# Kernel optimization log

Hardware: AMD Instinct MI355X
Metric: run time of the kernel (lower is better)

Reference implementation:

```python
import jax, jax.numpy as jnp
import numpy as np

N_SUB = 60000   # nodes in current subgraph (rows of fnode/agraph/subnode)
M = 120000      # total messages (directed edges)
K = 8           # max neighbors per node/message
H = 128         # hidden_size
IN = 256        # input_size (fmess feature dim)
FD = 128        # node_fdim
DEPTH = 2       # rnn depth (sparse_forward iterations)
NUM_NODES = 65536


def setup_inputs() -> dict:
    key = jax.random.key(0)
    ks = jax.random.split(key, 12)
    s = 0.05
    def w(k, shape):
        return jax.random.normal(k, shape, jnp.float32) * s
    return {
        "fnode": jax.random.normal(ks[0], (N_SUB, FD), jnp.float32),
        "fmess": jax.random.normal(ks[1], (M, IN), jnp.float32),
        "agraph": jax.random.randint(ks[2], (N_SUB, K), 0, M, dtype=jnp.int32),
        "bgraph": jax.random.randint(ks[3], (M, K), 0, M, dtype=jnp.int32),
        "h_in": jax.random.normal(ks[4], (M, H), jnp.float32),
        "c_in": jax.random.normal(ks[5], (M, H), jnp.float32),
        "submess": jnp.arange(N_SUB, dtype=jnp.int32),
        "subnode": jnp.arange(N_SUB, dtype=jnp.int32),
        "num_nodes": NUM_NODES,
        # tree-LSTM gate weights, stored [in_dim, out_dim]
        "Wi": w(ks[6], (IN + H, H)), "bi": jnp.zeros((H,), jnp.float32),
        "Wo": w(ks[7], (IN + H, H)), "bo": jnp.zeros((H,), jnp.float32),
        "Wf": w(ks[8], (IN + H, H)), "bf": jnp.zeros((H,), jnp.float32),
        "Wu": w(ks[9], (IN + H, H)), "bu": jnp.zeros((H,), jnp.float32),
        # node readout W_o: Linear(node_fdim + hidden -> hidden) + ReLU (+ Dropout = eval no-op)
        "Wn": w(ks[10], (FD + H, H)), "bn": jnp.zeros((H,), jnp.float32),
    }


def _lstm_cell(x, h_nei, c_nei, Wi, bi, Wo, bo, Wf, bf, Wu, bu):
    # x: [S, IN]; h_nei, c_nei: [S, K, H]  (hgraph-style child-sum tree LSTM)
    h_sum = h_nei.sum(axis=1)                         # [S, H]
    z = jnp.concatenate([x, h_sum], axis=-1)          # [S, IN+H]
    i = jax.nn.sigmoid(z @ Wi + bi)
    o = jax.nn.sigmoid(z @ Wo + bo)
    u = jnp.tanh(z @ Wu + bu)
    # per-neighbor forget gate: sigmoid(cat([x_expand, h_nei]) @ Wf + bf),
    # split the matmul so we never materialize the [S, K, IN+H] concat
    d_in = x.shape[1]
    fx = x @ Wf[:d_in] + bf                           # [S, H]
    f = jax.nn.sigmoid(fx[:, None, :] + h_nei @ Wf[d_in:])  # [S, K, H]
    c = i * u + (f * c_nei).sum(axis=1)
    h = o * jnp.tanh(c)
    return h, c


def reference(fnode, fmess, agraph, bgraph, h_in, c_in, submess, subnode, num_nodes,
              Wi, bi, Wo, bo, Wf, bf, Wu, bu, Wn, bn):
    # LSTM.sparse_forward: zero state at submess rows, then iteratively update them
    mask = jnp.ones((h_in.shape[0],), h_in.dtype).at[submess].set(0.0)
    h = h_in * mask[:, None]
    c = c_in * mask[:, None]
    x_sub = fmess[submess]       # [S, IN]
    bg_sub = bgraph[submess]     # [S, K] message-neighbor ids
    for _ in range(DEPTH):
        h_nei = h[bg_sub]        # [S, K, H] gather
        c_nei = c[bg_sub]
        sub_h, sub_c = _lstm_cell(x_sub, h_nei, c_nei, Wi, bi, Wo, bo, Wf, bf, Wu, bu)
        h = h.at[submess].set(sub_h)   # index_scatter
        c = c.at[submess].set(sub_c)
    # node update: gather incoming messages, sum, Linear + ReLU (dropout inactive at eval)
    nei_message = h[agraph].sum(axis=1)                      # [N_SUB, H]
    node_hiddens = jnp.concatenate([fnode, nei_message], axis=-1)
    node_hiddens = jax.nn.relu(node_hiddens @ Wn + bn)       # [N_SUB, H]
    node_buf = jnp.zeros((num_nodes, node_hiddens.shape[1]), node_hiddens.dtype)
    node_buf = node_buf.at[subnode].set(node_hiddens)        # index_scatter into full buffer
    return node_buf, h, c
```

## Files before the change

### kernel.cpp

```cpp
#include <hip/hip_runtime.h>
#include <cstdint>
#include <cstddef>

#define Hc   128
#define INc  256
#define Kc   8
#define HP   136
#define HSP  136
#define EPH  136
#define ZP2  264

typedef unsigned short ushortT;
typedef __attribute__((ext_vector_type(8))) short bf16x8;
typedef __attribute__((ext_vector_type(4))) float f32x4;
typedef __attribute__((ext_vector_type(4))) unsigned short us4;
typedef __attribute__((ext_vector_type(8))) unsigned short us8;

__device__ __forceinline__ float fsig(float x) {
  return __builtin_amdgcn_rcpf(1.f + __expf(-x));
}
__device__ __forceinline__ float ftanh(float x) {
  float e = __expf(2.f * fminf(x, 15.f));
  return (e - 1.f) * __builtin_amdgcn_rcpf(e + 1.f);
}
__device__ __forceinline__ ushortT f2bf(float f) {
  unsigned u = __builtin_bit_cast(unsigned, f);
  unsigned r = (u + 0x7fffu + ((u >> 16) & 1u)) >> 16;
  return (ushortT)r;
}
__device__ __forceinline__ us4 f2bf4(float4 v) {
  us4 o; o[0] = f2bf(v.x); o[1] = f2bf(v.y); o[2] = f2bf(v.z); o[3] = f2bf(v.w);
  return o;
}
__device__ __forceinline__ float bf2f(ushortT u) {
  return __builtin_bit_cast(float, (unsigned)u << 16);
}

#define GATE_FRAGS (4*8*12*64)
#define WN_FRAGS   (8*8*64)

__global__ void marks_init(int* __restrict__ mark, int M, int* __restrict__ nmark, int NN) {
  int i = blockIdx.x * blockDim.x + threadIdx.x;
  if (i < M) mark[i] = -1;
  if (i < NN) nmark[i] = -1;
}

__global__ void set_repack(const int* __restrict__ submess, const int* __restrict__ subnode,
                           int S, int* __restrict__ mark, int* __restrict__ nmark,
                           const float* __restrict__ Wi, const float* __restrict__ Wo,
                           const float* __restrict__ Wu, const float* __restrict__ Wf,
                           const float* __restrict__ Wn, ushortT* __restrict__ pack, int SB) {
  if ((int)blockIdx.x < SB) {
    int i = blockIdx.x * 256 + threadIdx.x;
    if (i < S) { mark[submess[i]] = i; nmark[subnode[i]] = i; }
    return;
  }
  int idx = (blockIdx.x - SB) * 256 + threadIdx.x;
  if (idx < GATE_FRAGS) {
    int lane = idx & 63;
    int kt = (idx >> 6) % 12;
    int gc = idx / (64 * 12);
    int c = gc & 7, g = gc >> 3;
    const float* W = (g == 0) ? Wi : (g == 1) ? Wo : (g == 2) ? Wu : Wf;
    int k0 = kt * 32 + (lane >> 4) * 8;
    int col = c * 16 + (lane & 15);
    ushortT* dst = pack + (size_t)idx * 8;
    #pragma unroll
    for (int j = 0; j < 8; ++j) dst[j] = f2bf(W[(size_t)(k0 + j) * Hc + col]);
  } else if (idx < GATE_FRAGS + WN_FRAGS) {
    int i2 = idx - GATE_FRAGS;
    int lane = i2 & 63;
    int kt = (i2 >> 6) & 7;
    int c = i2 >> 9;
    int k0 = kt * 32 + (lane >> 4) * 8;
    int col = c * 16 + (lane & 15);
    ushortT* dst = pack + (size_t)GATE_FRAGS * 8 + (size_t)i2 * 8;
    #pragma unroll
    for (int j = 0; j < 8; ++j) dst[j] = f2bf(Wn[(size_t)(k0 + j) * Hc + col]);
  }
}

__device__ __forceinline__ const bf16x8* wh_frag(const ushortT* pack, int g, int cw, int kf, int lane) {
  return (const bf16x8*)&pack[(size_t)(((g * 8 + cw) * 12 + (8 + kf)) * 64 + lane) * 8];
}

__global__ __launch_bounds__(256) void stage_xg(
    const float* __restrict__ h_in, const float* __restrict__ c_in,
    const int* __restrict__ mark,
    float* __restrict__ h_out, float* __restrict__ c_out,
    ushortT* __restrict__ H16x, ushortT* __restrict__ C16x, ushortT* __restrict__ Hf16x,
    const float* __restrict__ fmess, const int* __restrict__ submess,
    const ushortT* __restrict__ pack,
    const float* __restrict__ bi, const float* __restrict__ bo,
    const float* __restrict__ bu, const float* __restrict__ bfb,
    ushortT* __restrict__ Xg, int M, int S, int stageBlocks)
{
  __shared__ __align__(16) ushortT xs[16 * ZP2];
  __shared__ int msr[16];
  const int t = threadIdx.x;

  if ((int)blockIdx.x < stageBlocks) {
    if (blockIdx.x == 0 && t < 48) {
      int arr = t >> 4, cp = t & 15;
      ushortT* dst = (arr == 0) ? H16x : (arr == 1) ? C16x : Hf16x;
      us8 z;
      #pragma unroll
      for (int e = 0; e < 8; ++e) z[e] = 0;
      *(us8*)&dst[(size_t)(M + S) * Hc + cp * 8] = z;
    }
    long total = (long)M * 16;
    for (long idx = (long)blockIdx.x * 256 + t; idx < total; idx += (long)stageBlocks * 256) {
      long j = idx >> 4;
      int cp = (int)(idx & 15);
      if (mark[j] >= 0) continue;
      const float4* h4 = (const float4*)(h_in + (size_t)j * Hc);
      const float4* c4 = (const float4*)(c_in + (size_t)j * Hc);
      float4 a0 = h4[cp * 2], a1 = h4[cp * 2 + 1];
      float4 b0 = c4[cp * 2], b1 = c4[cp * 2 + 1];
      ((float4*)(h_out + (size_t)j * Hc))[cp * 2] = a0;
      ((float4*)(h_out + (size_t)j * Hc))[cp * 2 + 1] = a1;
      ((float4*)(c_out + (size_t)j * Hc))[cp * 2] = b0;
      ((float4*)(c_out + (size_t)j * Hc))[cp * 2 + 1] = b1;
      *(us4*)&H16x[(size_t)j * Hc + cp * 8]     = f2bf4(a0);
      *(us4*)&H16x[(size_t)j * Hc + cp * 8 + 4] = f2bf4(a1);
      *(us4*)&C16x[(size_t)j * Hc + cp * 8]     = f2bf4(b0);
      *(us4*)&C16x[(size_t)j * Hc + cp * 8 + 4] = f2bf4(b1);
    }
    return;
  }

  const int row0 = (blockIdx.x - stageBlocks) * 16;
  if (t < 16) msr[t] = (row0 + t < S) ? submess[row0 + t] : -1;
  __syncthreads();
  {
    int r = t >> 4, cp = t & 15;
    int ms = msr[r];
    const float4* xr = (ms >= 0) ? (const float4*)(fmess + (size_t)ms * INc) : nullptr;
    #pragma unroll
    for (int q = 0; q < 4; ++q) {
      int slot = cp + q * 16;
      float4 v;
      if (xr) v = xr[slot]; else { v.x = v.y = v.z = v.w = 0.f; }
      *(us4*)&xs[r * ZP2 + slot * 4] = f2bf4(v);
    }
  }
  __syncthreads();

  const int w = t >> 6, lane = t & 63, lg = lane >> 4, cl = lane & 15;
  f32x4 acc[8];
  #pragma unroll
  for (int i = 0; i < 8; ++i) acc[i] = (f32x4){0.f, 0.f, 0.f, 0.f};
  const ushortT* zr = &xs[cl * ZP2 + lg * 8];
  #pragma unroll
  for (int kt = 0; kt < 8; ++kt) {
    bf16x8 a = *(const bf16x8*)&zr[kt * 32];
    #pragma unroll
    for (int c = 0; c < 8; ++c) {
      bf16x8 b = *(const bf16x8*)&pack[(size_t)(((w * 8 + c) * 12 + kt) * 64 + lane) * 8];
      acc[c] = __builtin_amdgcn_mfma_f32_16x16x32_bf16(a, b, acc[c], 0, 0, 0);
    }
  }
  const float* bias = (w == 0) ? bi : (w == 1) ? bo : (w == 2) ? bu : bfb;
  #pragma unroll
  for (int c = 0; c < 8; ++c) {
    int col = c * 16 + cl;
    float bv = bias[col];
    #pragma unroll
    for (int reg = 0; reg < 4; ++reg) {
      int s = row0 + lg * 4 + reg;
      if (s < S) Xg[(size_t)s * 512 + w * 128 + col] = f2bf(acc[c][reg] + bv);
    }
  }
}

__global__ __launch_bounds__(256) void hf_rows0(
    const ushortT* __restrict__ H16x, const int* __restrict__ mark,
    const ushortT* __restrict__ pack, ushortT* __restrict__ Hf16x, int M)
{
  __shared__ __align__(16) ushortT zh[16 * HP];
  __shared__ int mk[16];
  const int t = threadIdx.x;
  const int row0 = blockIdx.x * 16;

  if (t < 16) mk[t] = (row0 + t < M) ? mark[row0 + t] : 0;
  __syncthreads();
  {
    int r = t >> 4, cp = t & 15;
    us8 v;
    #pragma unroll
    for (int e = 0; e < 8; ++e) v[e] = 0;
    if (mk[r] < 0) v = *(const us8*)&H16x[(size_t)(row0 + r) * Hc + cp * 8];
    *(us8*)&zh[r * HP + cp * 8] = v;
  }
  __syncthreads();

  const int w = t >> 6, lane = t & 63, lg = lane >> 4, cl = lane & 15;
  f32x4 acc0 = (f32x4){0.f,0.f,0.f,0.f}, acc1 = acc0;
  const ushortT* zr = &zh[cl * HP + lg * 8];
  #pragma unroll
  for (int kf = 0; kf < 4; ++kf) {
    bf16x8 a = *(const bf16x8*)&zr[kf * 32];
    acc0 = __builtin_amdgcn_mfma_f32_16x16x32_bf16(a, *wh_frag(pack, 3, w*2+0, kf, lane), acc0, 0, 0, 0);
    acc1 = __builtin_amdgcn_mfma_f32_16x16x32_bf16(a, *wh_frag(pack, 3, w*2+1, kf, lane), acc1, 0, 0, 0);
  }
  #pragma unroll
  for (int half = 0; half < 2; ++half) {
    int col = (w * 2 + half) * 16 + cl;
    f32x4 a_ = half ? acc1 : acc0;
    #pragma unroll
    for (int reg = 0; reg < 4; ++reg) {
      int row = lg * 4 + reg;
      if (mk[row] < 0) Hf16x[(size_t)(row0 + row) * Hc + col] = f2bf(a_[reg]);
    }
  }
}

template<int MODE>
__global__ __launch_bounds__(256) void lstm8(
    const int* __restrict__ submess, const int* __restrict__ bgraph,
    const int* __restrict__ mark,
    ushortT* H16x, ushortT* C16x, ushortT* Hf16x,
    const ushortT* __restrict__ Xg, const ushortT* __restrict__ pack,
    ushortT* hsumNS, ushortT* cpartNS,
    float* __restrict__ dstH, float* __restrict__ dstC, int S, int M)
{
  __shared__ __align__(16) ushortT zs[16 * HSP];
  __shared__ __align__(16) ushortT pih[16 * EPH];
  __shared__ __align__(16) ushortT poh[16 * EPH];
  __shared__ __align__(16) ushortT puh[16 * EPH];
  __shared__ int nbj[16][Kc];
  __shared__ int msrow[16];

  const int t = threadIdx.x;
  const int row0 = blockIdx.x * 16;
  const int DUMMY = M + S;

  if (t < 128) {
    int r = t >> 3, k = t & 7;
    int s = row0 + r;
    int ms = (s < S) ? submess[s] : -1;
    if (k == 0) msrow[r] = ms;
    int j = DUMMY;
    if (ms >= 0) {
      int jj = bgraph[(size_t)ms * Kc + k];
      int m = mark[jj];
      j = (MODE == 0) ? (m >= 0 ? DUMMY : jj) : (m >= 0 ? M + m : DUMMY);
    }
    nbj[r][k] = j;
  }
  __syncthreads();

  {
    int r = t >> 4, cp = t & 15;
    int spos = row0 + r;
    float sum[8] = {0.f,0.f,0.f,0.f,0.f,0.f,0.f,0.f};
    if (MODE == 1 && spos < S) {
      us8 hs = *(const us8*)&hsumNS[(size_t)spos * Hc + cp * 8];
      #pragma unroll
      for (int e = 0; e < 8; ++e) sum[e] = bf2f(hs[e]);
    }
    #pragma unroll
    for (int k = 0; k < Kc; ++k) {
      int j = nbj[r][k];
      us8 v = *(const us8*)&H16x[(size_t)j * Hc + cp * 8];
      #pragma unroll
      for (int e = 0; e < 8; ++e) sum[e] += bf2f(v[e]);
    }
    us4 o0, o1;
    #pragma unroll
    for (int e = 0; e < 4; ++e) { o0[e] = f2bf(sum[e]); o1[e] = f2bf(sum[4 + e]); }
    *(us4*)&zs[r * HSP + cp * 8] = o0;
    *(us4*)&zs[r * HSP + cp * 8 + 4] = o1;
    if (MODE == 0 && spos < S) {
      *(us4*)&hsumNS[(size_t)spos * Hc + cp * 8] = o0;
      *(us4*)&hsumNS[(size_t)spos * Hc + cp * 8 + 4] = o1;
    }
  }
  __syncthreads();

  const int w = t >> 6, lane = t & 63, lg = lane >> 4, cl = lane & 15;

  f32x4 acc[6];
  #pragma unroll
  for (int i = 0; i < 6; ++i) acc[i] = (f32x4){0.f, 0.f, 0.f, 0.f};
  const ushortT* zrow = &zs[cl * HSP + lg * 8];
  #pragma unroll
  for (int kf = 0; kf < 4; ++kf) {
    bf16x8 a = *(const bf16x8*)&zrow[kf * 32];
    #pragma unroll
    for (int g = 0; g < 3; ++g)
      #pragma unroll
      for (int half = 0; half < 2; ++half)
        acc[g * 2 + half] = __builtin_amdgcn_mfma_f32_16x16x32_bf16(
            a, *wh_frag(pack, g, w * 2 + half, kf, lane), acc[g * 2 + half], 0, 0, 0);
  }

  #pragma unroll
  for (int half = 0; half < 2; ++half) {
    int col = (w * 2 + half) * 16 + cl;
    #pragma unroll
    for (int reg = 0; reg < 4; ++reg) {
      int row = lg * 4 + reg;
      pih[row * EPH + col] = f2bf(acc[0 + half][reg]);
      poh[row * EPH + col] = f2bf(acc[2 + half][reg]);
      puh[row * EPH + col] = f2bf(acc[4 + half][reg]);
    }
  }
  __syncthreads();

  {
    int r = t >> 4, cc = t & 15;
    int ms = msrow[r];
    int spos = row0 + r;
    const ushortT* xgr = Xg + (size_t)spos * 512 + cc * 8;
    us8 xi8 = *(const us8*)&xgr[0];
    us8 xo8 = *(const us8*)&xgr[128];
    us8 xu8 = *(const us8*)&xgr[256];
    us8 xf8 = *(const us8*)&xgr[384];
    us8 pi8 = *(const us8*)&pih[r * EPH + cc * 8];
    us8 po8 = *(const us8*)&poh[r * EPH + cc * 8];
    us8 pu8 = *(const us8*)&puh[r * EPH + cc * 8];
    float fx[8], ovv[8], iu[8], cn[8];
    #pragma unroll
    for (int e = 0; e < 8; ++e) {
      float iv = fsig(bf2f(xi8[e]) + bf2f(pi8[e]));
      float uv = ftanh(bf2f(xu8[e]) + bf2f(pu8[e]));
      ovv[e] = fsig(bf2f(xo8[e]) + bf2f(po8[e]));
      fx[e] = bf2f(xf8[e]);
      iu[e] = iv * uv;
      cn[e] = 0.f;
    }
    #pragma unroll
    for (int k = 0; k < Kc; ++k) {
      int j = nbj[r][k];
      us8 hf8 = *(const us8*)&Hf16x[(size_t)j * Hc + cc * 8];
      us8 cn8 = *(const us8*)&C16x[(size_t)j * Hc + cc * 8];
      #pragma unroll
      for (int e = 0; e < 8; ++e)
        cn[e] = fmaf(fsig(fx[e] + bf2f(hf8[e])), bf2f(cn8[e]), cn[e]);
    }
    float cacc[8];
    if (MODE == 1 && spos < S) {
      us8 cp8 = *(const us8*)&cpartNS[(size_t)spos * Hc + cc * 8];
      #pragma unroll
      for (int e = 0; e < 8; ++e) cacc[e] = iu[e] + cn[e] + bf2f(cp8[e]);
    } else {
      #pragma unroll
      for (int e = 0; e < 8; ++e) cacc[e] = iu[e] + cn[e];
    }
    float hv[8];
    #pragma unroll
    for (int e = 0; e < 8; ++e) hv[e] = ovv[e] * ftanh(cacc[e]);

    if (MODE == 0) {
      us8 h8, c8, cn16;
      #pragma unroll
      for (int e = 0; e < 8; ++e) {
        h8[e] = (spos < S) ? f2bf(hv[e]) : (ushortT)0;
        c8[e] = f2bf(cacc[e]);
        cn16[e] = f2bf(cn[e]);
      }
      if (spos < S) {
        *(us8*)&H16x[(size_t)(M + spos) * Hc + cc * 8] = h8;
        *(us8*)&C16x[(size_t)(M + spos) * Hc + cc * 8] = c8;
        *(us8*)&cpartNS[(size_t)spos * Hc + cc * 8] = cn16;
      }
      *(us4*)&zs[r * HSP + cc * 8]     = (us4){h8[0], h8[1], h8[2], h8[3]};
      *(us4*)&zs[r * HSP + cc * 8 + 4] = (us4){h8[4], h8[5], h8[6], h8[7]};
    } else {
      if (ms >= 0) {
        float* dh = dstH + (size_t)ms * Hc + cc * 8;
        float* dc = dstC + (size_t)ms * Hc + cc * 8;
        *(float4*)&dh[0] = *(float4*)&hv[0];
        *(float4*)&dh[4] = *(float4*)&hv[4];
        *(float4*)&dc[0] = *(float4*)&cacc[0];
        *(float4*)&dc[4] = *(float4*)&cacc[4];
      }
    }
  }

  if (MODE == 0) {
    __syncthreads();
    f32x4 a0 = (f32x4){0.f,0.f,0.f,0.f}, a1 = a0;
    const ushortT* zr2 = &zs[cl * HSP + lg * 8];
    #pragma unroll
    for (int kf = 0; kf < 4; ++kf) {
      bf16x8 a = *(const bf16x8*)&zr2[kf * 32];
      a0 = __builtin_amdgcn_mfma_f32_16x16x32_bf16(a, *wh_frag(pack, 3, w*2+0, kf, lane), a0, 0, 0, 0);
      a1 = __builtin_amdgcn_mfma_f32_16x16x32_bf16(a, *wh_frag(pack, 3, w*2+1, kf, lane), a1, 0, 0, 0);
    }
    #pragma unroll
    for (int half = 0; half < 2; ++half) {
      int col = (w * 2 + half) * 16 + cl;
      f32x4 a_ = half ? a1 : a0;
      #pragma unroll
      for (int reg = 0; reg < 4; ++reg) {
        int sp = row0 + lg * 4 + reg;
        if (sp < S) Hf16x[(size_t)(M + sp) * Hc + col] = f2bf(a_[reg]);
      }
    }
  }
}

__global__ __launch_bounds__(256) void readout_zero(
    const float* __restrict__ fnode, const int* __restrict__ agraph,
    const int* __restrict__ subnode, const float* __restrict__ h_out,
    const ushortT* __restrict__ H16x, const int* __restrict__ mark,
    const int* __restrict__ nmark,
    const ushortT* __restrict__ packWn, const float* __restrict__ bn,
    float* __restrict__ node_buf, int Nsub, int num_nodes, int NB, int ZB)
{
  __shared__ __align__(16) ushortT z2[16 * ZP2];
  __shared__ int orow[16];
  __shared__ int jn[16][Kc];

  const int t = threadIdx.x;

  if ((int)blockIdx.x >= NB) {
    long total = (long)num_nodes * 16;
    float4 z; z.x = z.y = z.z = z.w = 0.f;
    for (long idx = (long)(blockIdx.x - NB) * 256 + t; idx < total; idx += (long)ZB * 256) {
      long v = idx >> 4;
      int cp = (int)(idx & 15);
      if (nmark[v] < 0) {
        ((float4*)(node_buf + (size_t)v * Hc))[cp * 2] = z;
        ((float4*)(node_buf + (size_t)v * Hc))[cp * 2 + 1] = z;
      }
    }
    return;
  }

  const int row0 = blockIdx.x * 16;
  if (t < 16) orow[t] = (row0 + t < Nsub) ? subnode[row0 + t] : -1;
  if (t >= 64 && t < 64 + 128) {
    int i = t - 64, r = i >> 3, k = i & 7;
    int v = row0 + r;
    int j = 0;
    if (v < Nsub) {
      j = agraph[(size_t)v * Kc + k];
      if (mark[j] >= 0) j = ~j;
    }
    jn[r][k] = j;
  }
  {
    int r = t >> 4, cp = t & 15;
    int v = row0 + r;
    const float4* fr = (v < Nsub) ? (const float4*)(fnode + (size_t)v * Hc) : nullptr;
    float4 v0, v1; v0.x = v0.y = v0.z = v0.w = 0.f; v1 = v0;
    if (fr) { v0 = fr[cp]; v1 = fr[cp + 16]; }
    *(us4*)&z2[r * ZP2 + cp * 4] = f2bf4(v0);
    *(us4*)&z2[r * ZP2 + 64 + cp * 4] = f2bf4(v1);
  }
  __syncthreads();
  {
    int r = t >> 4, cp = t & 15;
    float sum[8] = {0.f,0.f,0.f,0.f,0.f,0.f,0.f,0.f};
    #pragma unroll
    for (int k = 0; k < Kc; ++k) {
      int je = jn[r][k];
      if (je < 0) {
        int j = ~je;
        float4 p0 = ((const float4*)(h_out + (size_t)j * Hc))[cp * 2];
        float4 p1 = ((const float4*)(h_out + (size_t)j * Hc))[cp * 2 + 1];
        sum[0] += p0.x; sum[1] += p0.y; sum[2] += p0.z; sum[3] += p0.w;
        sum[4] += p1.x; sum[5] += p1.y; sum[6] += p1.z; sum[7] += p1.w;
      } else {
        us8 v = *(const us8*)&H16x[(size_t)je * Hc + cp * 8];
        #pragma unroll
        for (int e = 0; e < 8; ++e) sum[e] += bf2f(v[e]);
      }
    }
    us4 o0, o1;
    #pragma unroll
    for (int e = 0; e < 4; ++e) { o0[e] = f2bf(sum[e]); o1[e] = f2bf(sum[4 + e]); }
    *(us4*)&z2[r * ZP2 + Hc + cp * 8] = o0;
    *(us4*)&z2[r * ZP2 + Hc + cp * 8 + 4] = o1;
  }
  __syncthreads();

  const int w = t >> 6, lane = t & 63;
  const int lg = lane >> 4, cl = lane & 15;

  f32x4 acc0 = (f32x4){0.f,0.f,0.f,0.f};
  f32x4 acc1 = (f32x4){0.f,0.f,0.f,0.f};
  const ushortT* zr = &z2[cl * ZP2 + lg * 8];
  #pragma unroll
  for (int kt = 0; kt < 8; ++kt) {
    bf16x8 a = *(const bf16x8*)&zr[kt * 32];
    bf16x8 b0 = *(const bf16x8*)&packWn[(size_t)(((w * 2 + 0) * 8 + kt) * 64 + lane) * 8];
    bf16x8 b1 = *(const bf16x8*)&packWn[(size_t)(((w * 2 + 1) * 8 + kt) * 64 + lane) * 8];
    acc0 = __builtin_amdgcn_mfma_f32_16x16x32_bf16(a, b0, acc0, 0, 0, 0);
    acc1 = __builtin_amdgcn_mfma_f32_16x16x32_bf16(a, b1, acc1, 0, 0, 0);
  }
  #pragma unroll
  for (int half = 0; half < 2; ++half) {
    int col = (w * 2 + half) * 16 + cl;
    float bnv = bn[col];
    f32x4 a_ = half ? acc1 : acc0;
    #pragma unroll
    for (int reg = 0; reg < 4; ++reg) {
      int row = lg * 4 + reg;
      int o = orow[row];
      if (o >= 0) node_buf[(size_t)o * Hc + col] = fmaxf(a_[reg] + bnv, 0.f);
    }
  }
}

extern "C" void kernel_launch(void* const* d_in, const int* in_sizes, int n_in,
                              void* d_out, int out_size, void* d_ws, size_t ws_size,
                              hipStream_t stream) {
  const float* fnode   = (const float*)d_in[0];
  const float* fmess   = (const float*)d_in[1];
  const int*   agraph  = (const int*)d_in[2];
  const int*   bgraph  = (const int*)d_in[3];
  const float* h_in    = (const float*)d_in[4];
  const float* c_in    = (const float*)d_in[5];
  const int*   submess = (const int*)d_in[6];
  const int*   subnode = (const int*)d_in[7];
  const float* Wi = (const float*)d_in[9];
  const float* bi = (const float*)d_in[10];
  const float* Wo = (const float*)d_in[11];
  const float* bo = (const float*)d_in[12];
  const float* Wf = (const float*)d_in[13];
  const float* bf_ = (const float*)d_in[14];
  const float* Wu = (const float*)d_in[15];
  const float* bu = (const float*)d_in[16];
  const float* Wn = (const float*)d_in[17];
  const float* bn = (const float*)d_in[18];

  const int S    = in_sizes[6];
  const int Nsub = in_sizes[2] / Kc;
  const int M    = in_sizes[4] / Hc;
  const int num_nodes = out_size / Hc - 2 * M;

  float* node_buf = (float*)d_out;
  float* h_out = node_buf + (size_t)num_nodes * Hc;
  float* c_out = h_out + (size_t)M * Hc;

  const int lblocks = (S + 15) / 16;

  int* mark = (int*)d_ws;
  size_t off = (((size_t)M * sizeof(int)) + 255) & ~(size_t)255;
  int* nmark = (int*)((char*)d_ws + off);
  off += (((size_t)num_nodes * sizeof(int)) + 255) & ~(size_t)255;
  ushortT* pack = (ushortT*)((char*)d_ws + off);
  off += (((size_t)(GATE_FRAGS + WN_FRAGS) * 8 * sizeof(ushortT)) + 255) & ~(size_t)255;
  size_t shadow_bytes = (((size_t)(M + S + 1) * Hc * sizeof(ushortT)) + 255) & ~(size_t)255;
  ushortT* Hf16x = (ushortT*)((char*)d_ws + off); off += shadow_bytes;
  ushortT* C16x  = (ushortT*)((char*)d_ws + off); off += shadow_bytes;
  ushortT* H16x  = (ushortT*)((char*)d_ws + off); off += shadow_bytes;
  ushortT* Xg    = (ushortT*)((char*)d_ws + off);
  ushortT* packWn = pack + (size_t)GATE_FRAGS * 8;
  ushortT* cpartNS = (ushortT*)node_buf;
  ushortT* hsumNS  = cpartNS + (size_t)S * Hc;

  int initN = (M > num_nodes) ? M : num_nodes;
  hipLaunchKernelGGL(marks_init, dim3((initN + 255) / 256), dim3(256), 0, stream,
                     mark, M, nmark, num_nodes);
  {
    int SB = (S + 255) / 256;
    int RB = (GATE_FRAGS + WN_FRAGS + 255) / 256;
    hipLaunchKernelGGL(set_repack, dim3(SB + RB), dim3(256), 0, stream,
                       submess, subnode, S, mark, nmark, Wi, Wo, Wu, Wf, Wn, pack, SB);
  }
  {
    int stageBlocks = 1024;
    hipLaunchKernelGGL(stage_xg, dim3(stageBlocks + lblocks), dim3(256), 0, stream,
                       h_in, c_in, mark, h_out, c_out, H16x, C16x, Hf16x,
                       fmess, submess, pack, bi, bo, bu, bf_, Xg, M, S, stageBlocks);
  }
  hipLaunchKernelGGL(hf_rows0, dim3((M + 15) / 16), dim3(256), 0, stream,
                     H16x, mark, pack, Hf16x, M);
  hipLaunchKernelGGL(lstm8<0>, dim3(lblocks), dim3(256), 0, stream,
      submess, bgraph, mark, H16x, C16x, Hf16x, Xg, pack,
      hsumNS, cpartNS, h_out, c_out, S, M);
  hipLaunchKernelGGL(lstm8<1>, dim3(lblocks), dim3(256), 0, stream,
      submess, bgraph, mark, H16x, C16x, Hf16x, Xg, pack,
      hsumNS, cpartNS, h_out, c_out, S, M);
  {
    int NB = (Nsub + 15) / 16;
    int ZB = 512;
    hipLaunchKernelGGL(readout_zero, dim3(NB + ZB), dim3(256), 0, stream,
        fnode, agraph, subnode, h_out, H16x, mark, nmark, packWn, bn,
        node_buf, Nsub, num_nodes, NB, ZB);
  }
}
```

Measured before the change: 288.8 us.

## Fuse state staging with Hf projection kernel and widen bf16 stores

Merges the h/c staging pass and the hf_rows0 projection into one kernel. Each block stages 16 message rows, converts them to bf16 and runs the forget-gate h projection straight from shared memory. This removes one launch and the re-read of H16x from global memory. Several paired 4-wide bf16 stores are also merged into single 8-wide stores. In exchange, the grid-stride staging loop becomes one block per 16 rows, which means many more blocks.

```diff
diff --git a/kernel.cpp b/kernel.cpp
--- a/kernel.cpp
+++ b/kernel.cpp
@@ -30,6 +30,12 @@
 }
 __device__ __forceinline__ us4 f2bf4(float4 v) {
   us4 o; o[0] = f2bf(v.x); o[1] = f2bf(v.y); o[2] = f2bf(v.z); o[3] = f2bf(v.w);
+  return o;
+}
+__device__ __forceinline__ us8 f2bf8(float4 a, float4 b) {
+  us8 o;
+  o[0] = f2bf(a.x); o[1] = f2bf(a.y); o[2] = f2bf(a.z); o[3] = f2bf(a.w);
+  o[4] = f2bf(b.x); o[5] = f2bf(b.y); o[6] = f2bf(b.z); o[7] = f2bf(b.w);
   return o;
 }
 __device__ __forceinline__ float bf2f(ushortT u) {
@@ -84,35 +90,90 @@
   return (const bf16x8*)&pack[(size_t)(((g * 8 + cw) * 12 + (8 + kf)) * 64 + lane) * 8];
 }
 
-__global__ __launch_bounds__(256) void stage_xg(
+__global__ __launch_bounds__(256) void xg_stage_hf(
+    const float* __restrict__ fmess, const int* __restrict__ submess,
+    const ushortT* __restrict__ pack,
+    const float* __restrict__ bi, const float* __restrict__ bo,
+    const float* __restrict__ bu, const float* __restrict__ bfb,
+    ushortT* __restrict__ Xg,
     const float* __restrict__ h_in, const float* __restrict__ c_in,
     const int* __restrict__ mark,
     float* __restrict__ h_out, float* __restrict__ c_out,
     ushortT* __restrict__ H16x, ushortT* __restrict__ C16x, ushortT* __restrict__ Hf16x,
-    const float* __restrict__ fmess, const int* __restrict__ submess,
-    const ushortT* __restrict__ pack,
-    const float* __restrict__ bi, const float* __restrict__ bo,
-    const float* __restrict__ bu, const float* __restrict__ bfb,
-    ushortT* __restrict__ Xg, int M, int S, int stageBlocks)
+    int M, int S, int XB)
 {
-  __shared__ __align__(16) ushortT xs[16 * ZP2];
-  __shared__ int msr[16];
+  __shared__ __align__(16) unsigned char pool[16 * ZP2 * 2];
+  __shared__ int aux[16];
   const int t = threadIdx.x;
-
-  if ((int)blockIdx.x < stageBlocks) {
-    if (blockIdx.x == 0 && t < 48) {
-      int arr = t >> 4, cp = t & 15;
-      ushortT* dst = (arr == 0) ? H16x : (arr == 1) ? C16x : Hf16x;
-      us8 z;
-      #pragma unroll
-      for (int e = 0; e < 8; ++e) z[e] = 0;
-      *(us8*)&dst[(size_t)(M + S) * Hc + cp * 8] = z;
-    }
-    long total = (long)M * 16;
-    for (long idx = (long)blockIdx.x * 256 + t; idx < total; idx += (long)stageBlocks * 256) {
-      long j = idx >> 4;
-      int cp = (int)(idx & 15);
-      if (mark[j] >= 0) continue;
+  const int w = t >> 6, lane = t & 63, lg = lane >> 4, cl = lane & 15;
+
+  if ((int)blockIdx.x < XB) {
+    ushortT* xs = (ushortT*)pool;
+    const int row0 = blockIdx.x * 16;
+    if (t < 16) aux[t] = (row0 + t < S) ? submess[row0 + t] : -1;
+    __syncthreads();
+    {
+      int r = t >> 4, cp = t & 15;
+      int ms = aux[r];
+      const float4* xr = (ms >= 0) ? (const float4*)(fmess + (size_t)ms * INc) : nullptr;
+      #pragma unroll
+      for (int q = 0; q < 4; ++q) {
+        int slot = cp + q * 16;
+        float4 v;
+        if (xr) v = xr[slot]; else { v.x = v.y = v.z = v.w = 0.f; }
+        *(us4*)&xs[r * ZP2 + slot * 4] = f2bf4(v);
+      }
+    }
+    __syncthreads();
+
+    f32x4 acc[8];
+    #pragma unroll
+    for (int i = 0; i < 8; ++i) acc[i] = (f32x4){0.f, 0.f, 0.f, 0.f};
+    const ushortT* zr = &xs[cl * ZP2 + lg * 8];
+    #pragma unroll
+    for (int kt = 0; kt < 8; ++kt) {
+      bf16x8 a = *(const bf16x8*)&zr[kt * 32];
+      #pragma unroll
+      for (int c = 0; c < 8; ++c) {
+        bf16x8 b = *(const bf16x8*)&pack[(size_t)(((w * 8 + c) * 12 + kt) * 64 + lane) * 8];
+        acc[c] = __builtin_amdgcn_mfma_f32_16x16x32_bf16(a, b, acc[c], 0, 0, 0);
+      }
+    }
+    const float* bias = (w == 0) ? bi : (w == 1) ? bo : (w == 2) ? bu : bfb;
+    #pragma unroll
+    for (int c = 0; c < 8; ++c) {
+      int col = c * 16 + cl;
+      float bv = bias[col];
+      #pragma unroll
+      for (int reg = 0; reg < 4; ++reg) {
+        int s = row0 + lg * 4 + reg;
+        if (s < S) Xg[(size_t)s * 512 + w * 128 + col] = f2bf(acc[c][reg] + bv);
+      }
+    }
+    return;
+  }
+
+  ushortT* zh = (ushortT*)pool;
+  int* mk = aux;
+  const int row0 = (blockIdx.x - XB) * 16;
+
+  if (blockIdx.x == XB && t < 48) {
+    int arr = t >> 4, cp = t & 15;
+    ushortT* dst = (arr == 0) ? H16x : (arr == 1) ? C16x : Hf16x;
+    us8 z;
+    #pragma unroll
+    for (int e = 0; e < 8; ++e) z[e] = 0;
+    *(us8*)&dst[(size_t)(M + S) * Hc + cp * 8] = z;
+  }
+  if (t < 16) mk[t] = (row0 + t < M) ? mark[row0 + t] : 0;
+  __syncthreads();
+  {
+    int r = t >> 4, cp = t & 15;
+    int j = row0 + r;
+    us8 hz;
+    #pragma unroll
+    for (int e = 0; e < 8; ++e) hz[e] = 0;
+    if (j < M && mk[r] < 0) {
       const float4* h4 = (const float4*)(h_in + (size_t)j * Hc);
       const float4* c4 = (const float4*)(c_in + (size_t)j * Hc);
       float4 a0 = h4[cp * 2], a1 = h4[cp * 2 + 1];
@@ -121,80 +182,15 @@
       ((float4*)(h_out + (size_t)j * Hc))[cp * 2 + 1] = a1;
       ((float4*)(c_out + (size_t)j * Hc))[cp * 2] = b0;
       ((float4*)(c_out + (size_t)j * Hc))[cp * 2 + 1] = b1;
-      *(us4*)&H16x[(size_t)j * Hc + cp * 8]     = f2bf4(a0);
-      *(us4*)&H16x[(size_t)j * Hc + cp * 8 + 4] = f2bf4(a1);
-      *(us4*)&C16x[(size_t)j * Hc + cp * 8]     = f2bf4(b0);
-      *(us4*)&C16x[(size_t)j * Hc + cp * 8 + 4] = f2bf4(b1);
-    }
-    return;
-  }
-
-  const int row0 = (blockIdx.x - stageBlocks) * 16;
-  if (t < 16) msr[t] = (row0 + t < S) ? submess[row0 + t] : -1;
-  __syncthreads();
-  {
-    int r = t >> 4, cp = t & 15;
-    int ms = msr[r];
-    const float4* xr = (ms >= 0) ? (const float4*)(fmess + (size_t)ms * INc) : nullptr;
-    #pragma unroll
-    for (int q = 0; q < 4; ++q) {
-      int slot = cp + q * 16;
-      float4 v;
-      if (xr) v = xr[slot]; else { v.x = v.y = v.z = v.w = 0.f; }
-      *(us4*)&xs[r * ZP2 + slot * 4] = f2bf4(v);
-    }
-  }
-  __syncthreads();
-
-  const int w = t >> 6, lane = t & 63, lg = lane >> 4, cl = lane & 15;
-  f32x4 acc[8];
-  #pragma unroll
-  for (int i = 0; i < 8; ++i) acc[i] = (f32x4){0.f, 0.f, 0.f, 0.f};
-  const ushortT* zr = &xs[cl * ZP2 + lg * 8];
-  #pragma unroll
-  for (int kt = 0; kt < 8; ++kt) {
-    bf16x8 a = *(const bf16x8*)&zr[kt * 32];
-    #pragma unroll
-    for (int c = 0; c < 8; ++c) {
-      bf16x8 b = *(const bf16x8*)&pack[(size_t)(((w * 8 + c) * 12 + kt) * 64 + lane) * 8];
-      acc[c] = __builtin_amdgcn_mfma_f32_16x16x32_bf16(a, b, acc[c], 0, 0, 0);
-    }
-  }
-  const float* bias = (w == 0) ? bi : (w == 1) ? bo : (w == 2) ? bu : bfb;
-  #pragma unroll
-  for (int c = 0; c < 8; ++c) {
-    int col = c * 16 + cl;
-    float bv = bias[col];
-    #pragma unroll
-    for (int reg = 0; reg < 4; ++reg) {
-      int s = row0 + lg * 4 + reg;
-      if (s < S) Xg[(size_t)s * 512 + w * 128 + col] = f2bf(acc[c][reg] + bv);
-    }
-  }
-}
-
-__global__ __launch_bounds__(256) void hf_rows0(
-    const ushortT* __restrict__ H16x, const int* __restrict__ mark,
-    const ushortT* __restrict__ pack, ushortT* __restrict__ Hf16x, int M)
-{
-  __shared__ __align__(16) ushortT zh[16 * HP];
-  __shared__ int mk[16];
-  const int t = threadIdx.x;
-  const int row0 = blockIdx.x * 16;
-
-  if (t < 16) mk[t] = (row0 + t < M) ? mark[row0 + t] : 0;
-  __syncthreads();
-  {
-    int r = t >> 4, cp = t & 15;
-    us8 v;
-    #pragma unroll
-    for (int e = 0; e < 8; ++e) v[e] = 0;
-    if (mk[r] < 0) v = *(const us8*)&H16x[(size_t)(row0 + r) * Hc + cp * 8];
-    *(us8*)&zh[r * HP + cp * 8] = v;
-  }
-  __syncthreads();
-
-  const int w = t >> 6, lane = t & 63, lg = lane >> 4, cl = lane & 15;
+      us8 h8 = f2bf8(a0, a1);
+      *(us8*)&H16x[(size_t)j * Hc + cp * 8] = h8;
+      *(us8*)&C16x[(size_t)j * Hc + cp * 8] = f2bf8(b0, b1);
+      hz = h8;
+    }
+    *(us8*)&zh[r * HP + cp * 8] = hz;
+  }
+  __syncthreads();
+
   f32x4 acc0 = (f32x4){0.f,0.f,0.f,0.f}, acc1 = acc0;
   const ushortT* zr = &zh[cl * HP + lg * 8];
   #pragma unroll
@@ -210,7 +206,8 @@
     #pragma unroll
     for (int reg = 0; reg < 4; ++reg) {
       int row = lg * 4 + reg;
-      if (mk[row] < 0) Hf16x[(size_t)(row0 + row) * Hc + col] = f2bf(a_[reg]);
+      if (row0 + row < M && mk[row] < 0)
+        Hf16x[(size_t)(row0 + row) * Hc + col] = f2bf(a_[reg]);
     }
   }
 }
@@ -266,15 +263,12 @@
       #pragma unroll
       for (int e = 0; e < 8; ++e) sum[e] += bf2f(v[e]);
     }
-    us4 o0, o1;
-    #pragma unroll
-    for (int e = 0; e < 4; ++e) { o0[e] = f2bf(sum[e]); o1[e] = f2bf(sum[4 + e]); }
-    *(us4*)&zs[r * HSP + cp * 8] = o0;
-    *(us4*)&zs[r * HSP + cp * 8 + 4] = o1;
-    if (MODE == 0 && spos < S) {
-      *(us4*)&hsumNS[(size_t)spos * Hc + cp * 8] = o0;
-      *(us4*)&hsumNS[(size_t)spos * Hc + cp * 8 + 4] = o1;
-    }
+    us8 o8;
+    #pragma unroll
+    for (int e = 0; e < 8; ++e) o8[e] = f2bf(sum[e]);
+    *(us8*)&zs[r * HSP + cp * 8] = o8;
+    if (MODE == 0 && spos < S)
+      *(us8*)&hsumNS[(size_t)spos * Hc + cp * 8] = o8;
   }
   __syncthreads();
 
@@ -365,8 +359,7 @@
         *(us8*)&C16x[(size_t)(M + spos) * Hc + cc * 8] = c8;
         *(us8*)&cpartNS[(size_t)spos * Hc + cc * 8] = cn16;
       }
-      *(us4*)&zs[r * HSP + cc * 8]     = (us4){h8[0], h8[1], h8[2], h8[3]};
-      *(us4*)&zs[r * HSP + cc * 8 + 4] = (us4){h8[4], h8[5], h8[6], h8[7]};
+      *(us8*)&zs[r * HSP + cc * 8] = h8;
     } else {
       if (ms >= 0) {
         float* dh = dstH + (size_t)ms * Hc + cc * 8;
@@ -470,11 +463,10 @@
         for (int e = 0; e < 8; ++e) sum[e] += bf2f(v[e]);
       }
     }
-    us4 o0, o1;
-    #pragma unroll
-    for (int e = 0; e < 4; ++e) { o0[e] = f2bf(sum[e]); o1[e] = f2bf(sum[4 + e]); }
-    *(us4*)&z2[r * ZP2 + Hc + cp * 8] = o0;
-    *(us4*)&z2[r * ZP2 + Hc + cp * 8 + 4] = o1;
+    us8 o8;
+    #pragma unroll
+    for (int e = 0; e < 8; ++e) o8[e] = f2bf(sum[e]);
+    *(us8*)&z2[r * ZP2 + Hc + cp * 8] = o8;
   }
   __syncthreads();
 
@@ -564,13 +556,13 @@
                        submess, subnode, S, mark, nmark, Wi, Wo, Wu, Wf, Wn, pack, SB);
   }
   {
-    int stageBlocks = 1024;
-    hipLaunchKernelGGL(stage_xg, dim3(stageBlocks + lblocks), dim3(256), 0, stream,
+    int XB = lblocks;
+    int SB2 = (M + 15) / 16;
+    hipLaunchKernelGGL(xg_stage_hf, dim3(XB + SB2), dim3(256), 0, stream,
+                       fmess, submess, pack, bi, bo, bu, bf_, Xg,
                        h_in, c_in, mark, h_out, c_out, H16x, C16x, Hf16x,
-                       fmess, submess, pack, bi, bo, bu, bf_, Xg, M, S, stageBlocks);
-  }
-  hipLaunchKernelGGL(hf_rows0, dim3((M + 15) / 16), dim3(256), 0, stream,
-                     H16x, mark, pack, Hf16x, M);
+                       M, S, XB);
+  }
   hipLaunchKernelGGL(lstm8<0>, dim3(lblocks), dim3(256), 0, stream,
       submess, bgraph, mark, H16x, C16x, Hf16x, Xg, pack,
       hsumNS, cpartNS, h_out, c_out, S, M);
```

After: 285.4 us. About the same (-1.2%).
